# Kernel optimization log

Hardware: AMD Instinct MI355X
Metric: run time of the kernel (lower is better)

Reference implementation:

```python
import jax, jax.numpy as jnp
import numpy as np

N_NODES = 100000
N_EDGES = 500000
IN_DIM, HID, N_CLS = 128, 512, 40


def gcn_conv(x, W, b, src, dst, num_nodes):
    # PyG GCNConv: h = x W; add self-loops; norm = d^-1/2[src] * d^-1/2[dst];
    # out[dst] += norm * h[src]; out += bias
    h = x @ W  # [N, out_dim]
    ones = jnp.ones(src.shape[0], dtype=x.dtype)
    deg = jax.ops.segment_sum(ones, dst, num_segments=num_nodes)  # in-degree incl self-loops
    dinv = jnp.where(deg > 0, jax.lax.rsqrt(deg), 0.0)
    norm = dinv[src] * dinv[dst]  # [E]
    msgs = h[src] * norm[:, None]  # [E, out_dim] gather + scale
    out = jax.ops.segment_sum(msgs, dst, num_segments=num_nodes)
    return out + b


def setup_inputs() -> dict:
    key = jax.random.key(0)
    k1, k2, k3, k4, k5, k6 = jax.random.split(key, 6)
    x = jax.random.normal(k1, (N_NODES, IN_DIM), dtype=jnp.float32)
    edge_index = jax.random.randint(k2, (2, N_EDGES), 0, N_NODES, dtype=jnp.int32)
    # Glorot-ish params
    W1 = jax.random.normal(k3, (IN_DIM, HID), dtype=jnp.float32) * (1.0 / np.sqrt(IN_DIM))
    b1 = jnp.zeros((HID,), dtype=jnp.float32)
    W2 = jax.random.normal(k4, (HID, N_CLS), dtype=jnp.float32) * (1.0 / np.sqrt(HID))
    b2 = jnp.zeros((N_CLS,), dtype=jnp.float32)
    return {"x": x, "edge_index": edge_index, "W1": W1, "b1": b1, "W2": W2, "b2": b2}


def reference(x, edge_index, W1, b1, W2, b2):
    n = x.shape[0]
    # add self-loops once, shared by both conv layers
    loop = jnp.arange(n, dtype=edge_index.dtype)
    src = jnp.concatenate([edge_index[0], loop])
    dst = jnp.concatenate([edge_index[1], loop])
    h = gcn_conv(x, W1, b1, src, dst, n)
    h = jax.nn.relu(h)
    # dropout is identity in eval mode (reference computed in eval)
    h = gcn_conv(h, W2, b2, src, dst, n)
    return jax.nn.log_softmax(h, axis=1)
```

## Files before the change

kernel.cpp:

```cpp
#include <hip/hip_runtime.h>
#include <cstdint>
#include <cstddef>

#define N_NODES 100000
#define N_EDGES 500000
#define IN_DIM  128
#define HID     512
#define N_CLS   40
#define N_SBLK  ((N_NODES + 255) / 256)
#define N_CNTB  ((N_EDGES + 255) / 256)
#define N_XBFB  12500
#define N_G1B   12500
#define N_PREPB 352

typedef short bf16x8 __attribute__((ext_vector_type(8)));
typedef float f32x4 __attribute__((ext_vector_type(4)));

__device__ inline unsigned short f2bf(float f) {
  unsigned u = __float_as_uint(f);
  u = u + 0x7fffu + ((u >> 16) & 1u);
  return (unsigned short)(u >> 16);
}
__device__ inline float blo(unsigned u) { return __uint_as_float(u << 16); }
__device__ inline float bhi(unsigned u) { return __uint_as_float(u & 0xffff0000u); }

__global__ __launch_bounds__(256) void k_zero(int* __restrict__ cnt, unsigned* __restrict__ flags) {
  int i = blockIdx.x * 256 + threadIdx.x;
  if (i < N_NODES) cnt[i] = 0;
  if (i == 0) flags[0] = 0;
}

__global__ __launch_bounds__(256) void k_count(const int* __restrict__ dst, int* __restrict__ cnt,
                                               int* __restrict__ rank) {
  int e = blockIdx.x * 256 + threadIdx.x;
  if (e < N_EDGES) rank[e] = atomicAdd(&cnt[dst[e]], 1);
}

__global__ __launch_bounds__(256) void k_scan(const int* __restrict__ cnt, unsigned* __restrict__ flags,
                                              int* __restrict__ offsets, float* __restrict__ dinv) {
  __shared__ int s[256];
  __shared__ int base_sh;
  int b = blockIdx.x;
  int i = b * 256 + threadIdx.x;
  int v = (i < N_NODES) ? cnt[i] : 0;
  s[threadIdx.x] = v;
  __syncthreads();
  #pragma unroll
  for (int off = 1; off < 256; off <<= 1) {
    int t = (threadIdx.x >= off) ? s[threadIdx.x - off] : 0;
    __syncthreads();
    s[threadIdx.x] += t;
    __syncthreads();
  }
  int incl = s[threadIdx.x];
  if (threadIdx.x == 0)
    base_sh = (int)atomicAdd(&flags[0], (unsigned)s[255]);
  __syncthreads();
  if (i < N_NODES) {
    int excl = base_sh + incl - v;
    offsets[i] = excl;
    dinv[i]    = rsqrtf((float)(v + 1));
  }
}

__global__ __launch_bounds__(256) void k_fill_xbf(const int* __restrict__ src, const int* __restrict__ dst,
                                                  const int* __restrict__ rank, const int* __restrict__ offsets,
                                                  const float* __restrict__ dinv, int2* __restrict__ epair,
                                                  const float* __restrict__ x, uint2* __restrict__ xb2) {
  int b = blockIdx.x;
  if (b < N_CNTB) {
    int e = b * 256 + threadIdx.x;
    if (e >= N_EDGES) return;
    int s = src[e], d = dst[e];
    int pos = offsets[d] + rank[e];
    float nrm = dinv[s] * dinv[d];
    epair[pos] = make_int2(s, __float_as_int(nrm));
  } else {
    int t = (b - N_CNTB) * 256 + threadIdx.x;
    float4 v = ((const float4*)x)[t];
    uint2 o;
    o.x = (unsigned)f2bf(v.x) | ((unsigned)f2bf(v.y) << 16);
    o.y = (unsigned)f2bf(v.z) | ((unsigned)f2bf(v.w) << 16);
    xb2[t] = o;
  }
}

__global__ __launch_bounds__(256) void k_gather1(const uint2* __restrict__ xb, const int2* __restrict__ ep,
                                                 const int* __restrict__ offsets, const int* __restrict__ cnt,
                                                 const float* __restrict__ dinv, uint2* __restrict__ z1,
                                                 const float* __restrict__ W1, const float* __restrict__ W2,
                                                 unsigned short* __restrict__ W1F, unsigned short* __restrict__ W2F) {
  int b = blockIdx.x;
  if (b >= N_G1B) {
    int t = (b - N_G1B) * 256 + threadIdx.x;
    if (t < 65536) {
      int j = t & 7, lane = (t >> 3) & 63, rest = t >> 9;
      int s2 = rest & 3, c = rest >> 2;
      int k = s2 * 32 + (lane >> 4) * 8 + j;
      int n = c * 16 + (lane & 15);
      W1F[t] = f2bf(W1[k * HID + n]);
    } else {
      int u = t - 65536;
      int j = u & 7, lane = (u >> 3) & 63, rest = u >> 9;
      int ct = rest % 3, gk = rest / 3;
      int k = gk * 32 + (lane >> 4) * 8 + j;
      int col = ct * 16 + (lane & 15);
      W2F[u] = (col < N_CLS) ? f2bf(W2[k * N_CLS + col]) : (unsigned short)0;
    }
    return;
  }
  int lane = threadIdx.x & 63, h = lane >> 5, l = lane & 31;
  int d = b * 8 + (threadIdx.x >> 6) * 2 + h;
  int start = offsets[d], end = start + cnt[d];
  float dd = dinv[d], sl = dd * dd;
  uint2 su = xb[(size_t)d * 32 + l];
  float a0 = sl * blo(su.x), a1 = sl * bhi(su.x), a2 = sl * blo(su.y), a3 = sl * bhi(su.y);
  float p0a = 0.f, p1a = 0.f, p2a = 0.f, p3a = 0.f;
  float q0a = 0.f, q1a = 0.f, q2a = 0.f, q3a = 0.f;
  float r0a = 0.f, r1a = 0.f, r2a = 0.f, r3a = 0.f;

  int i = start;
  for (; i + 3 < end; i += 4) {
    int2 e0 = ep[i], e1 = ep[i + 1], e2 = ep[i + 2], e3 = ep[i + 3];
    uint2 r0 = xb[(size_t)e0.x * 32 + l];
    uint2 r1 = xb[(size_t)e1.x * 32 + l];
    uint2 r2 = xb[(size_t)e2.x * 32 + l];
    uint2 r3 = xb[(size_t)e3.x * 32 + l];
    float n0 = __int_as_float(e0.y), n1 = __int_as_float(e1.y);
    float n2 = __int_as_float(e2.y), n3 = __int_as_float(e3.y);
    a0  += n0 * blo(r0.x); a1  += n0 * bhi(r0.x); a2  += n0 * blo(r0.y); a3  += n0 * bhi(r0.y);
    p0a += n1 * blo(r1.x); p1a += n1 * bhi(r1.x); p2a += n1 * blo(r1.y); p3a += n1 * bhi(r1.y);
    q0a += n2 * blo(r2.x); q1a += n2 * bhi(r2.x); q2a += n2 * blo(r2.y); q3a += n2 * bhi(r2.y);
    r0a += n3 * blo(r3.x); r1a += n3 * bhi(r3.x); r2a += n3 * blo(r3.y); r3a += n3 * bhi(r3.y);
  }
  for (; i < end; ++i) {
    int2 e0 = ep[i];
    uint2 r0 = xb[(size_t)e0.x * 32 + l];
    float n0 = __int_as_float(e0.y);
    a0 += n0 * blo(r0.x); a1 += n0 * bhi(r0.x); a2 += n0 * blo(r0.y); a3 += n0 * bhi(r0.y);
  }
  a0 += p0a + q0a + r0a;
  a1 += p1a + q1a + r1a;
  a2 += p2a + q2a + r2a;
  a3 += p3a + q3a + r3a;
  uint2 o;
  o.x = (unsigned)f2bf(a0) | ((unsigned)f2bf(a1) << 16);
  o.y = (unsigned)f2bf(a2) | ((unsigned)f2bf(a3) << 16);
  z1[(size_t)d * 32 + l] = o;
}

#define HS_STRIDE 56
__global__ __launch_bounds__(64) void k_fused_mfma(const unsigned short* __restrict__ z1b,
                                                   const unsigned short* __restrict__ W1F,
                                                   const float* __restrict__ b1,
                                                   const unsigned short* __restrict__ W2F,
                                                   unsigned short* __restrict__ Pb) {
  __shared__ unsigned short Hs[32 * HS_STRIDE];
  const int lane = threadIdx.x;
  const int c16  = lane & 15, quad = lane >> 4;
  const int odd  = c16 & 1;
  const int mbase = blockIdx.x * 32;

  bf16x8 afrag[2][4];
  #pragma unroll
  for (int t = 0; t < 2; ++t) {
    int mrow = mbase + t * 16 + c16;
    const bf16x8* arow = (const bf16x8*)(z1b + (size_t)mrow * IN_DIM + quad * 8);
    afrag[t][0] = arow[0];
    afrag[t][1] = arow[4];
    afrag[t][2] = arow[8];
    afrag[t][3] = arow[12];
  }

  f32x4 pacc[2][3];
  #pragma unroll
  for (int t = 0; t < 2; ++t)
    #pragma unroll
    for (int ct = 0; ct < 3; ++ct) pacc[t][ct] = (f32x4){0.f, 0.f, 0.f, 0.f};

  const bf16x8* w1f = (const bf16x8*)W1F;
  const bf16x8* w2f = (const bf16x8*)W2F;
  unsigned short* hs = Hs;

  for (int g = 0; g < 16; ++g) {
    #pragma unroll
    for (int nt = 0; nt < 2; ++nt) {
      int c = g * 2 + nt;
      bf16x8 bp0 = w1f[(c * 4 + 0) * 64 + lane];
      bf16x8 bp1 = w1f[(c * 4 + 1) * 64 + lane];
      bf16x8 bp2 = w1f[(c * 4 + 2) * 64 + lane];
      bf16x8 bp3 = w1f[(c * 4 + 3) * 64 + lane];
      f32x4 h[2];
      #pragma unroll
      for (int t = 0; t < 2; ++t) h[t] = (f32x4){0.f, 0.f, 0.f, 0.f};
      #pragma unroll
      for (int t = 0; t < 2; ++t) h[t] = __builtin_amdgcn_mfma_f32_16x16x32_bf16(afrag[t][0], bp0, h[t], 0, 0, 0);
      #pragma unroll
      for (int t = 0; t < 2; ++t) h[t] = __builtin_amdgcn_mfma_f32_16x16x32_bf16(afrag[t][1], bp1, h[t], 0, 0, 0);
      #pragma unroll
      for (int t = 0; t < 2; ++t) h[t] = __builtin_amdgcn_mfma_f32_16x16x32_bf16(afrag[t][2], bp2, h[t], 0, 0, 0);
      #pragma unroll
      for (int t = 0; t < 2; ++t) h[t] = __builtin_amdgcn_mfma_f32_16x16x32_bf16(afrag[t][3], bp3, h[t], 0, 0, 0);
      float bias = b1[c * 16 + c16];
      int colb = nt * 16 + (c16 & ~1);
      int rb0  = quad * 4 + (odd ? 2 : 0);
      #pragma unroll
      for (int t = 0; t < 2; ++t) {
        float v0 = fmaxf(h[t][0] + bias, 0.f);
        float v1 = fmaxf(h[t][1] + bias, 0.f);
        float v2 = fmaxf(h[t][2] + bias, 0.f);
        float v3 = fmaxf(h[t][3] + bias, 0.f);
        float o0 = __shfl_xor(v0, 1, 64);
        float o1 = __shfl_xor(v1, 1, 64);
        float o2 = __shfl_xor(v2, 1, 64);
        float o3 = __shfl_xor(v3, 1, 64);
        float lo0 = odd ? o2 : v0, hi0 = odd ? v2 : o0;
        float lo1 = odd ? o3 : v1, hi1 = odd ? v3 : o1;
        unsigned p0, p1;
        asm("v_cvt_pk_bf16_f32 %0, %1, %2" : "=v"(p0) : "v"(lo0), "v"(hi0));
        asm("v_cvt_pk_bf16_f32 %0, %1, %2" : "=v"(p1) : "v"(lo1), "v"(hi1));
        *(unsigned*)(hs + (t * 16 + rb0    ) * HS_STRIDE + colb) = p0;
        *(unsigned*)(hs + (t * 16 + rb0 + 1) * HS_STRIDE + colb) = p1;
      }
    }
    bf16x8 hf[2];
    #pragma unroll
    for (int t = 0; t < 2; ++t)
      hf[t] = *(const bf16x8*)(hs + (t * 16 + c16) * HS_STRIDE + quad * 8);
    #pragma unroll
    for (int ct = 0; ct < 3; ++ct) {
      bf16x8 bf = w2f[(g * 3 + ct) * 64 + lane];
      #pragma unroll
      for (int t = 0; t < 2; ++t)
        pacc[t][ct] = __builtin_amdgcn_mfma_f32_16x16x32_bf16(hf[t], bf, pacc[t][ct], 0, 0, 0);
    }
  }

  #pragma unroll
  for (int t = 0; t < 2; ++t) {
    int mrow0 = mbase + t * 16 + quad * 4;
    #pragma unroll
    for (int ct = 0; ct < 3; ++ct) {
      int col = ct * 16 + c16;
      if (col < N_CLS) {
        #pragma unroll
        for (int r = 0; r < 4; ++r) {
          int m = mrow0 + r;
          Pb[(size_t)m * N_CLS + col] = f2bf(pacc[t][ct][r]);
        }
      }
    }
  }
}

__global__ __launch_bounds__(256) void k_gather2_lsm(const uint2* __restrict__ Pu2,
                                                     const int2* __restrict__ ep,
                                                     const int* __restrict__ offsets, const int* __restrict__ cnt,
                                                     const float* __restrict__ dinv, const float* __restrict__ b2,
                                                     float* __restrict__ out) {
  int lane = threadIdx.x & 63, q = lane >> 4, l = lane & 15;
  int d = blockIdx.x * 16 + (threadIdx.x >> 6) * 4 + q;
  bool act = l < 10;
  int lc = act ? l : 0;
  int start = offsets[d], end = start + cnt[d];
  float dd = dinv[d], sl = dd * dd;

  uint2 su = Pu2[(size_t)d * 10 + lc];
  float a0 = sl * blo(su.x), a1 = sl * bhi(su.x), a2 = sl * blo(su.y), a3 = sl * bhi(su.y);
  float p0a = 0.f, p1a = 0.f, p2a = 0.f, p3a = 0.f;
  float q0a = 0.f, q1a = 0.f, q2a = 0.f, q3a = 0.f;
  float r0a = 0.f, r1a = 0.f, r2a = 0.f, r3a = 0.f;

  int i = start;
  for (; i + 3 < end; i += 4) {
    int2 e0 = ep[i], e1 = ep[i + 1], e2 = ep[i + 2], e3 = ep[i + 3];
    uint2 u0 = Pu2[(size_t)e0.x * 10 + lc];
    uint2 u1 = Pu2[(size_t)e1.x * 10 + lc];
    uint2 u2 = Pu2[(size_t)e2.x * 10 + lc];
    uint2 u3 = Pu2[(size_t)e3.x * 10 + lc];
    float n0 = __int_as_float(e0.y), n1 = __int_as_float(e1.y);
    float n2 = __int_as_float(e2.y), n3 = __int_as_float(e3.y);
    a0  += n0 * blo(u0.x); a1  += n0 * bhi(u0.x); a2  += n0 * blo(u0.y); a3  += n0 * bhi(u0.y);
    p0a += n1 * blo(u1.x); p1a += n1 * bhi(u1.x); p2a += n1 * blo(u1.y); p3a += n1 * bhi(u1.y);
    q0a += n2 * blo(u2.x); q1a += n2 * bhi(u2.x); q2a += n2 * blo(u2.y); q3a += n2 * bhi(u2.y);
    r0a += n3 * blo(u3.x); r1a += n3 * bhi(u3.x); r2a += n3 * blo(u3.y); r3a += n3 * bhi(u3.y);
  }
  for (; i < end; ++i) {
    int2 e0 = ep[i];
    uint2 u0 = Pu2[(size_t)e0.x * 10 + lc];
    float n0 = __int_as_float(e0.y);
    a0 += n0 * blo(u0.x); a1 += n0 * bhi(u0.x); a2 += n0 * blo(u0.y); a3 += n0 * bhi(u0.y);
  }

  float v0, v1, v2, v3;
  if (act) {
    float4 bb = ((const float4*)b2)[l];
    v0 = a0 + p0a + q0a + r0a + bb.x;
    v1 = a1 + p1a + q1a + r1a + bb.y;
    v2 = a2 + p2a + q2a + r2a + bb.z;
    v3 = a3 + p3a + q3a + r3a + bb.w;
  } else {
    v0 = v1 = v2 = v3 = -1e30f;
  }
  float m = fmaxf(fmaxf(v0, v1), fmaxf(v2, v3));
  #pragma unroll
  for (int off = 8; off > 0; off >>= 1) m = fmaxf(m, __shfl_xor(m, off, 64));
  float e = act ? (expf(v0 - m) + expf(v1 - m) + expf(v2 - m) + expf(v3 - m)) : 0.f;
  float s = e;
  #pragma unroll
  for (int off = 8; off > 0; off >>= 1) s += __shfl_xor(s, off, 64);
  float lse = m + logf(s);
  if (act) {
    float4 o = make_float4(v0 - lse, v1 - lse, v2 - lse, v3 - lse);
    ((float4*)(out + (size_t)d * N_CLS))[l] = o;
  }
}

extern "C" void kernel_launch(void* const* d_in, const int* in_sizes, int n_in,
                              void* d_out, int out_size, void* d_ws, size_t ws_size,
                              hipStream_t stream) {
  const float* x  = (const float*)d_in[0];
  const int*   ei = (const int*)d_in[1];
  const int*  src = ei;
  const int*  dst = ei + N_EDGES;
  const float* W1 = (const float*)d_in[2];
  const float* b1 = (const float*)d_in[3];
  const float* W2 = (const float*)d_in[4];
  const float* b2 = (const float*)d_in[5];
  float* out = (float*)d_out;

  float* dinv    = (float*)d_ws;
  int*   cnt     = (int*)(dinv + 131072);
  int*   offsets = cnt + 131072;
  unsigned* flags = (unsigned*)(offsets + 131072);
  int*   rank    = (int*)(flags + 1024);
  int2*  epair   = (int2*)(rank + 524288);
  uint2* xb2     = (uint2*)(epair + 524288);
  unsigned short* Pb = (unsigned short*)xb2;
  unsigned short* z1b = (unsigned short*)(xb2 + 3200000);
  unsigned short* W1F = z1b + (size_t)N_NODES * IN_DIM;
  unsigned short* W2F = W1F + HID * IN_DIM;

  k_zero    <<<N_SBLK, 256, 0, stream>>>(cnt, flags);
  k_count   <<<N_CNTB, 256, 0, stream>>>(dst, cnt, rank);
  k_scan    <<<N_SBLK, 256, 0, stream>>>(cnt, flags, offsets, dinv);
  k_fill_xbf<<<N_CNTB + N_XBFB, 256, 0, stream>>>(src, dst, rank, offsets, dinv, epair, x, xb2);
  k_gather1 <<<N_G1B + N_PREPB, 256, 0, stream>>>(xb2, epair, offsets, cnt, dinv, (uint2*)z1b,
                                                  W1, W2, W1F, W2F);
  k_fused_mfma<<<N_NODES / 32, 64, 0, stream>>>(z1b, W1F, b1, W2F, Pb);
  k_gather2_lsm<<<N_NODES / 16, 256, 0, stream>>>((const uint2*)Pb, epair, offsets, cnt, dinv, b2, out);
}
```

Before: 230.6 us.

## Compute transposed first GEMM so MFMA output feeds second GEMM from registers

Swaps the MFMA operand order so the first GEMM produces H transposed, and permutes the W1 fragment layout so each lane's accumulator values line up with the A-operand fragment layout of the second GEMM. The LDS round-trip, the cross-lane shuffles and the shared-memory staging buffer are removed, and H goes straight from registers into the second MFMA chain. Bias is loaded as float4 per lane, and all W1/W2 fragments for a group are loaded up front. The cost is higher register pressure and reliance on an exact fragment permutation for correctness.

```diff
diff --git a/kernel.cpp b/kernel.cpp
--- a/kernel.cpp
+++ b/kernel.cpp
@@ -95,15 +95,16 @@
     int t = (b - N_G1B) * 256 + threadIdx.x;
     if (t < 65536) {
       int j = t & 7, lane = (t >> 3) & 63, rest = t >> 9;
-      int s2 = rest & 3, c = rest >> 2;
-      int k = s2 * 32 + (lane >> 4) * 8 + j;
-      int n = c * 16 + (lane & 15);
-      W1F[t] = f2bf(W1[k * HID + n]);
+      int kfrag = rest & 3, c = rest >> 2;
+      int k = kfrag * 32 + ((lane >> 4) & 3) * 8 + j;
+      int i = lane & 15;
+      int h = (c >> 1) * 32 + (i >> 2) * 8 + (c & 1) * 4 + (i & 3);
+      W1F[t] = f2bf(W1[k * HID + h]);
     } else {
       int u = t - 65536;
       int j = u & 7, lane = (u >> 3) & 63, rest = u >> 9;
       int ct = rest % 3, gk = rest / 3;
-      int k = gk * 32 + (lane >> 4) * 8 + j;
+      int k = gk * 32 + ((lane >> 4) & 3) * 8 + j;
       int col = ct * 16 + (lane & 15);
       W2F[u] = (col < N_CLS) ? f2bf(W2[k * N_CLS + col]) : (unsigned short)0;
     }
@@ -149,16 +150,13 @@
   z1[(size_t)d * 32 + l] = o;
 }
 
-#define HS_STRIDE 56
 __global__ __launch_bounds__(64) void k_fused_mfma(const unsigned short* __restrict__ z1b,
                                                    const unsigned short* __restrict__ W1F,
                                                    const float* __restrict__ b1,
                                                    const unsigned short* __restrict__ W2F,
                                                    unsigned short* __restrict__ Pb) {
-  __shared__ unsigned short Hs[32 * HS_STRIDE];
   const int lane = threadIdx.x;
   const int c16  = lane & 15, quad = lane >> 4;
-  const int odd  = c16 & 1;
   const int mbase = blockIdx.x * 32;
 
   bf16x8 afrag[2][4];
@@ -180,59 +178,42 @@
 
   const bf16x8* w1f = (const bf16x8*)W1F;
   const bf16x8* w2f = (const bf16x8*)W2F;
-  unsigned short* hs = Hs;
+  const float4* b1v = (const float4*)b1;
 
   for (int g = 0; g < 16; ++g) {
-    #pragma unroll
-    for (int nt = 0; nt < 2; ++nt) {
-      int c = g * 2 + nt;
-      bf16x8 bp0 = w1f[(c * 4 + 0) * 64 + lane];
-      bf16x8 bp1 = w1f[(c * 4 + 1) * 64 + lane];
-      bf16x8 bp2 = w1f[(c * 4 + 2) * 64 + lane];
-      bf16x8 bp3 = w1f[(c * 4 + 3) * 64 + lane];
-      f32x4 h[2];
+    bf16x8 wa[8];
+    #pragma unroll
+    for (int f = 0; f < 8; ++f) wa[f] = w1f[(g * 8 + f) * 64 + lane];
+    bf16x8 wb[3];
+    #pragma unroll
+    for (int ct = 0; ct < 3; ++ct) wb[ct] = w2f[(g * 3 + ct) * 64 + lane];
+    float4 bb0 = b1v[g * 8 + quad * 2 + 0];
+    float4 bb1 = b1v[g * 8 + quad * 2 + 1];
+
+    #pragma unroll
+    for (int t = 0; t < 2; ++t) {
+      f32x4 h0 = (f32x4){0.f, 0.f, 0.f, 0.f};
+      f32x4 h1 = (f32x4){0.f, 0.f, 0.f, 0.f};
       #pragma unroll
-      for (int t = 0; t < 2; ++t) h[t] = (f32x4){0.f, 0.f, 0.f, 0.f};
+      for (int k = 0; k < 4; ++k)
+        h0 = __builtin_amdgcn_mfma_f32_16x16x32_bf16(wa[k], afrag[t][k], h0, 0, 0, 0);
       #pragma unroll
-      for (int t = 0; t < 2; ++t) h[t] = __builtin_amdgcn_mfma_f32_16x16x32_bf16(afrag[t][0], bp0, h[t], 0, 0, 0);
+      for (int k = 0; k < 4; ++k)
+        h1 = __builtin_amdgcn_mfma_f32_16x16x32_bf16(wa[4 + k], afrag[t][k], h1, 0, 0, 0);
+      float e0 = fmaxf(h0[0] + bb0.x, 0.f), e1 = fmaxf(h0[1] + bb0.y, 0.f);
+      float e2 = fmaxf(h0[2] + bb0.z, 0.f), e3 = fmaxf(h0[3] + bb0.w, 0.f);
+      float f0 = fmaxf(h1[0] + bb1.x, 0.f), f1 = fmaxf(h1[1] + bb1.y, 0.f);
+      float f2 = fmaxf(h1[2] + bb1.z, 0.f), f3 = fmaxf(h1[3] + bb1.w, 0.f);
+      unsigned q0, q1, q2, q3;
+      asm("v_cvt_pk_bf16_f32 %0, %1, %2" : "=v"(q0) : "v"(e0), "v"(e1));
+      asm("v_cvt_pk_bf16_f32 %0, %1, %2" : "=v"(q1) : "v"(e2), "v"(e3));
+      asm("v_cvt_pk_bf16_f32 %0, %1, %2" : "=v"(q2) : "v"(f0), "v"(f1));
+      asm("v_cvt_pk_bf16_f32 %0, %1, %2" : "=v"(q3) : "v"(f2), "v"(f3));
+      union { unsigned u[4]; bf16x8 v; } pa;
+      pa.u[0] = q0; pa.u[1] = q1; pa.u[2] = q2; pa.u[3] = q3;
       #pragma unroll
-      for (int t = 0; t < 2; ++t) h[t] = __builtin_amdgcn_mfma_f32_16x16x32_bf16(afrag[t][1], bp1, h[t], 0, 0, 0);
-      #pragma unroll
-      for (int t = 0; t < 2; ++t) h[t] = __builtin_amdgcn_mfma_f32_16x16x32_bf16(afrag[t][2], bp2, h[t], 0, 0, 0);
-      #pragma unroll
-      for (int t = 0; t < 2; ++t) h[t] = __builtin_amdgcn_mfma_f32_16x16x32_bf16(afrag[t][3], bp3, h[t], 0, 0, 0);
-      float bias = b1[c * 16 + c16];
-      int colb = nt * 16 + (c16 & ~1);
-      int rb0  = quad * 4 + (odd ? 2 : 0);
-      #pragma unroll
-      for (int t = 0; t < 2; ++t) {
-        float v0 = fmaxf(h[t][0] + bias, 0.f);
-        float v1 = fmaxf(h[t][1] + bias, 0.f);
-        float v2 = fmaxf(h[t][2] + bias, 0.f);
-        float v3 = fmaxf(h[t][3] + bias, 0.f);
-        float o0 = __shfl_xor(v0, 1, 64);
-        float o1 = __shfl_xor(v1, 1, 64);
-        float o2 = __shfl_xor(v2, 1, 64);
-        float o3 = __shfl_xor(v3, 1, 64);
-        float lo0 = odd ? o2 : v0, hi0 = odd ? v2 : o0;
-        float lo1 = odd ? o3 : v1, hi1 = odd ? v3 : o1;
-        unsigned p0, p1;
-        asm("v_cvt_pk_bf16_f32 %0, %1, %2" : "=v"(p0) : "v"(lo0), "v"(hi0));
-        asm("v_cvt_pk_bf16_f32 %0, %1, %2" : "=v"(p1) : "v"(lo1), "v"(hi1));
-        *(unsigned*)(hs + (t * 16 + rb0    ) * HS_STRIDE + colb) = p0;
-        *(unsigned*)(hs + (t * 16 + rb0 + 1) * HS_STRIDE + colb) = p1;
-      }
-    }
-    bf16x8 hf[2];
-    #pragma unroll
-    for (int t = 0; t < 2; ++t)
-      hf[t] = *(const bf16x8*)(hs + (t * 16 + c16) * HS_STRIDE + quad * 8);
-    #pragma unroll
-    for (int ct = 0; ct < 3; ++ct) {
-      bf16x8 bf = w2f[(g * 3 + ct) * 64 + lane];
-      #pragma unroll
-      for (int t = 0; t < 2; ++t)
-        pacc[t][ct] = __builtin_amdgcn_mfma_f32_16x16x32_bf16(hf[t], bf, pacc[t][ct], 0, 0, 0);
+      for (int ct = 0; ct < 3; ++ct)
+        pacc[t][ct] = __builtin_amdgcn_mfma_f32_16x16x32_bf16(pa.v, wb[ct], pacc[t][ct], 0, 0, 0);
     }
   }
 
```

After: 221.1 us. -4.1%, faster.
